# Kernel optimization log

Measured on AMD Instinct MI355X. Metric: run time of the kernel, lower is better.

The kernel has to match this reference:

```python
import jax, jax.numpy as jnp
import numpy as np

T, B, V, D, H, L, AH = 64, 128, 50000, 300, 300, 20, 300
EPS = 1e-8


def lstm_scan(x, Wih, Whh, b, h_dim):
    # x: [T, N, d_in]; PyTorch LSTM gate order i, f, g, o
    N = x.shape[1]

    def step(carry, xt):
        h, c = carry
        g = xt @ Wih.T + h @ Whh.T + b
        i, f, gg, o = jnp.split(g, 4, axis=-1)
        c = jax.nn.sigmoid(f) * c + jax.nn.sigmoid(i) * jnp.tanh(gg)
        h = jax.nn.sigmoid(o) * jnp.tanh(c)
        return (h, c), h

    init = (jnp.zeros((N, h_dim), x.dtype), jnp.zeros((N, h_dim), x.dtype))
    _, hs = jax.lax.scan(step, init, x)
    return hs  # [T, N, h_dim]


def mp_full(p, v, W):
    # p:[T,B,H], v:[B,H], W:[L,H] -> [T,B,L]; cos(W_l*p, W_l*v) via W^2 contraction
    W2 = W * W
    num = jnp.einsum('tbh,bh,lh->tbl', p, v, W2)
    pn = jnp.sqrt(jnp.einsum('tbh,lh->tbl', p * p, W2))
    vn = jnp.sqrt(jnp.einsum('bh,lh->bl', v * v, W2))
    return num / (pn * vn[None] + EPS)


def mp_elem(p, q, W):
    # p,q:[T,B,H] -> [T,B,L]
    W2 = W * W
    num = jnp.einsum('tbh,lh->tbl', p * q, W2)
    pn = jnp.sqrt(jnp.einsum('tbh,lh->tbl', p * p, W2))
    qn = jnp.sqrt(jnp.einsum('tbh,lh->tbl', q * q, W2))
    return num / (pn * qn + EPS)


def mp_pair(p, h, W):
    # p:[Tp,B,H], h:[Th,B,H] -> [Tp,Th,B,L]
    W2 = W * W
    num = jnp.einsum('tbh,sbh,lh->tsbl', p, h, W2)
    pn = jnp.sqrt(jnp.einsum('tbh,lh->tbl', p * p, W2))
    hn = jnp.sqrt(jnp.einsum('sbh,lh->sbl', h * h, W2))
    return num / (pn[:, None] * hn[None] + EPS)


def match_dir(p, h, v_full, Wf, Wm, Wa, Wma):
    full = mp_full(p, v_full, Wf)                       # full matching
    maxp = mp_pair(p, h, Wm).max(axis=1)                # maxpooling matching
    pn = p / (jnp.linalg.norm(p, axis=-1, keepdims=True) + EPS)
    hn = h / (jnp.linalg.norm(h, axis=-1, keepdims=True) + EPS)
    att = jnp.einsum('tbh,sbh->tsb', pn, hn)            # cosine attention
    w = att / (att.sum(axis=1, keepdims=True) + EPS)
    hmean = jnp.einsum('tsb,sbh->tbh', w, h)
    attm = mp_elem(p, hmean, Wa)                        # attentive matching
    idx = jnp.argmax(att, axis=1)                       # [Tp,B]
    hmax = h[idx, jnp.arange(h.shape[1])]               # [Tp,B,H]
    maxattm = mp_elem(p, hmax, Wma)                     # max-attentive matching
    return jnp.concatenate([full, maxp, attm, maxattm], axis=-1)


def multi_perspective(p_fw, p_bw, h_fw, h_bw, mp_W):
    m_fw = match_dir(p_fw, h_fw, h_fw[-1], mp_W[0], mp_W[1], mp_W[2], mp_W[3])
    m_bw = match_dir(p_bw, h_bw, h_bw[0], mp_W[4], mp_W[5], mp_W[6], mp_W[7])
    return jnp.concatenate([m_fw, m_bw], axis=-1)  # [T,B,8L]


def setup_inputs() -> dict:
    key = jax.random.key(0)
    ks = jax.random.split(key, 20)
    s = 0.05
    return {
        'premise': jax.random.randint(ks[0], (T, B), 0, V),
        'hypothesis': jax.random.randint(ks[1], (T, B), 0, V),
        'embed_W': jax.random.normal(ks[2], (V, D), jnp.float32),
        'cell_Wih': jax.random.normal(ks[3], (4 * H, D), jnp.float32) * s,
        'cell_Whh': jax.random.normal(ks[4], (4 * H, H), jnp.float32) * s,
        'cell_b': jax.random.normal(ks[5], (4 * H,), jnp.float32) * s,
        'mp_W': jax.random.normal(ks[6], (8, L, H), jnp.float32),
        'agg_Wih_f': jax.random.normal(ks[7], (4 * AH, 16 * L), jnp.float32) * s,
        'agg_Whh_f': jax.random.normal(ks[8], (4 * AH, AH), jnp.float32) * s,
        'agg_b_f': jax.random.normal(ks[9], (4 * AH,), jnp.float32) * s,
        'agg_Wih_b': jax.random.normal(ks[10], (4 * AH, 16 * L), jnp.float32) * s,
        'agg_Whh_b': jax.random.normal(ks[11], (4 * AH, AH), jnp.float32) * s,
        'agg_b_b': jax.random.normal(ks[12], (4 * AH,), jnp.float32) * s,
        'bn_gamma': jnp.ones((3, 2 * AH), jnp.float32),
        'bn_beta': jnp.zeros((3, 2 * AH), jnp.float32),
        'mlp_W1': jax.random.normal(ks[13], (2 * AH, 2 * AH), jnp.float32) * s,
        'mlp_b1': jax.random.normal(ks[14], (2 * AH,), jnp.float32) * s,
        'mlp_W2': jax.random.normal(ks[15], (2 * AH, 2 * AH), jnp.float32) * s,
        'mlp_b2': jax.random.normal(ks[16], (2 * AH,), jnp.float32) * s,
        'out_W': jax.random.normal(ks[17], (3, 2 * AH), jnp.float32) * s,
        'out_b': jax.random.normal(ks[18], (3,), jnp.float32) * s,
    }


def reference(premise, hypothesis, embed_W, cell_Wih, cell_Whh, cell_b, mp_W,
              agg_Wih_f, agg_Whh_f, agg_b_f, agg_Wih_b, agg_Whh_b, agg_b_b,
              bn_gamma, bn_beta, mlp_W1, mlp_b1, mlp_W2, mlp_b2, out_W, out_b):
    p = embed_W[premise]                      # [T,B,D]
    h = embed_W[hypothesis]                   # [T,B,D]
    comb = jnp.concatenate([p, h], axis=1)    # [T,2B,D] (premise|hypothesis along batch)
    hs_fw = lstm_scan(comb, cell_Wih, cell_Whh, cell_b, H)
    hs_bw = lstm_scan(comb[::-1], cell_Wih, cell_Whh, cell_b, H)[::-1]  # time-aligned
    p_fw, h_fw = hs_fw[:, :B], hs_fw[:, B:]
    p_bw, h_bw = hs_bw[:, :B], hs_bw[:, B:]
    m_ph = multi_perspective(p_fw, p_bw, h_fw, h_bw, mp_W)
    m_hp = multi_perspective(h_fw, h_bw, p_fw, p_bw, mp_W)
    m = jnp.concatenate([m_ph, m_hp], axis=-1)  # [T,B,16L]
    a_f = lstm_scan(m, agg_Wih_f, agg_Whh_f, agg_b_f, AH)[-1]
    a_b = lstm_scan(m[::-1], agg_Wih_b, agg_Whh_b, agg_b_b, AH)[-1]
    x = jnp.concatenate([a_f, a_b], axis=-1)    # [B, 2*AH]
    inv = np.float32(1.0 / np.sqrt(1.0 + 1e-5))  # eval-mode BN, running stats (0,1)
    bn = lambda z, i: bn_gamma[i] * z * inv + bn_beta[i]
    x = jax.nn.relu(bn(x, 0) @ mlp_W1.T + mlp_b1)
    x = jax.nn.relu(bn(x, 1) @ mlp_W2.T + mlp_b2)
    return bn(x, 2) @ out_W.T + out_b           # [B, 3]
```

## Files before the change

kernel.cpp:

```cpp
#include <hip/hip_runtime.h>
#include <cstddef>
#include <cstdint>
#include <math.h>

#define EPSF 1e-8f


typedef _Float16 half8v __attribute__((ext_vector_type(8)));
typedef float f32x4v __attribute__((ext_vector_type(4)));
union U4H8 { uint4 u; half8v h; _Float16 e[8]; };

__device__ __forceinline__ float fsig(float x) {
  float e = __expf(-x);
  return __builtin_amdgcn_rcpf(1.f + e);
}
__device__ __forceinline__ float ftanh(float x) {
  float e = __expf(-2.f * fabsf(x));
  float r = (1.f - e) * __builtin_amdgcn_rcpf(1.f + e);
  return copysignf(r, x);
}

__device__ __forceinline__ uint4 gld16(const uint4* p) {
  uint4 r;
  asm volatile("global_load_dwordx4 %0, %1, off" : "=v"(r) : "v"(p));
  return r;
}

#define GMM_LDS_BYTES (2 * (128 * 72 * 2) + 2 * (240 * 72 * 2))

__global__ __launch_bounds__(512, 1) void gemm_mfma_nt(
    const float* __restrict__ A, const float* __restrict__ B,
    const float* __restrict__ bias, float* __restrict__ C,
    int M, int K)
{
  extern __shared__ char smem[];
  _Float16* Ah = (_Float16*)smem;
  _Float16* Al = (_Float16*)(smem + 18432);
  _Float16* Bh = (_Float16*)(smem + 36864);
  _Float16* Bl = (_Float16*)(smem + 36864 + 34560);

  const int tid = threadIdx.x;
  const int wv = tid >> 6, lane = tid & 63;
  const int lm = lane & 15, lg = lane >> 4;
  const int mbase = blockIdx.y << 7;
  const int nbase = blockIdx.x * 240;

  f32x4v acc[15];
#pragma unroll
  for (int nt = 0; nt < 15; nt++) acc[nt] = (f32x4v){0.f, 0.f, 0.f, 0.f};

  const int nchunk = (K + 63) >> 6;
  for (int c = 0; c < nchunk; c++) {
    const int kc = c << 6;
    for (int e = tid; e < 2048; e += 512) {
      int row = e >> 4, q = e & 15;
      int k = kc + q * 4;
      const float* src = A + (size_t)(mbase + row) * K;
      float4 v = make_float4(0.f, 0.f, 0.f, 0.f);
      if (k + 4 <= K) {
        v = *(const float4*)(src + k);
      } else {
        if (k + 0 < K) v.x = src[k + 0];
        if (k + 1 < K) v.y = src[k + 1];
        if (k + 2 < K) v.z = src[k + 2];
        if (k + 3 < K) v.w = src[k + 3];
      }
      _Float16 hx = (_Float16)v.x, hy = (_Float16)v.y,
               hz = (_Float16)v.z, hw = (_Float16)v.w;
      _Float16* d = &Ah[row * 72 + q * 4];
      d[0] = hx; d[1] = hy; d[2] = hz; d[3] = hw;
      _Float16* dl = &Al[row * 72 + q * 4];
      dl[0] = (_Float16)(v.x - (float)hx); dl[1] = (_Float16)(v.y - (float)hy);
      dl[2] = (_Float16)(v.z - (float)hz); dl[3] = (_Float16)(v.w - (float)hw);
    }
    for (int e = tid; e < 3840; e += 512) {
      int row = e >> 4, q = e & 15;
      int k = kc + q * 4;
      const float* src = B + (size_t)(nbase + row) * K;
      float4 v = make_float4(0.f, 0.f, 0.f, 0.f);
      if (k + 4 <= K) {
        v = *(const float4*)(src + k);
      } else {
        if (k + 0 < K) v.x = src[k + 0];
        if (k + 1 < K) v.y = src[k + 1];
        if (k + 2 < K) v.z = src[k + 2];
        if (k + 3 < K) v.w = src[k + 3];
      }
      _Float16 hx = (_Float16)v.x, hy = (_Float16)v.y,
               hz = (_Float16)v.z, hw = (_Float16)v.w;
      _Float16* d = &Bh[row * 72 + q * 4];
      d[0] = hx; d[1] = hy; d[2] = hz; d[3] = hw;
      _Float16* dl = &Bl[row * 72 + q * 4];
      dl[0] = (_Float16)(v.x - (float)hx); dl[1] = (_Float16)(v.y - (float)hy);
      dl[2] = (_Float16)(v.z - (float)hz); dl[3] = (_Float16)(v.w - (float)hw);
    }
    __syncthreads();

#pragma unroll
    for (int kt = 0; kt < 2; kt++) {
      U4H8 ah, al;
      ah.u = *(const uint4*)&Ah[(wv * 16 + lm) * 72 + kt * 32 + lg * 8];
      al.u = *(const uint4*)&Al[(wv * 16 + lm) * 72 + kt * 32 + lg * 8];
#pragma unroll
      for (int nt = 0; nt < 15; nt++) {
        U4H8 bh, bl;
        bh.u = *(const uint4*)&Bh[(nt * 16 + lm) * 72 + kt * 32 + lg * 8];
        bl.u = *(const uint4*)&Bl[(nt * 16 + lm) * 72 + kt * 32 + lg * 8];
        acc[nt] = __builtin_amdgcn_mfma_f32_16x16x32_f16(ah.h, bh.h, acc[nt], 0, 0, 0);
        acc[nt] = __builtin_amdgcn_mfma_f32_16x16x32_f16(al.h, bh.h, acc[nt], 0, 0, 0);
        acc[nt] = __builtin_amdgcn_mfma_f32_16x16x32_f16(ah.h, bl.h, acc[nt], 0, 0, 0);
      }
    }
    __syncthreads();
  }

#pragma unroll
  for (int nt = 0; nt < 15; nt++) {
    int col = nbase + nt * 16 + lm;
    float bv = bias[col];
#pragma unroll
    for (int r = 0; r < 4; r++) {
      int m = mbase + wv * 16 + lg * 4 + r;
      C[(size_t)m * 1200 + col] = acc[nt][r] + bv;
    }
  }
}

__global__ __launch_bounds__(256) void permW_kernel(
    const float* __restrict__ W, const float* __restrict__ bias,
    float* __restrict__ Wp, float* __restrict__ bp, int K)
{
  int r = blockIdx.x;
  int gate = r & 3, u = r >> 2;
  int src = gate * 300 + u;
  const float* s = W + (size_t)src * K;
  float* d = Wp + (size_t)r * K;
  for (int c = threadIdx.x; c < K; c += 256) d[c] = s[c];
  if (threadIdx.x == 0) bp[r] = bias[src];
}

__global__ __launch_bounds__(256) void packB_kernel(
    const float* __restrict__ W0, const float* __restrict__ W1,
    const float* __restrict__ W2,
    uint4* __restrict__ T0, uint4* __restrict__ T1, uint4* __restrict__ T2)
{
  int i = blockIdx.x * 256 + threadIdx.x;
  if (i >= 48000) return;
  const float* W = (blockIdx.y == 0) ? W0 : (blockIdx.y == 1) ? W1 : W2;
  uint4* T = (blockIdx.y == 0) ? T0 : (blockIdx.y == 1) ? T1 : T2;
  int lane = i & 63;
  int tile = i >> 6;
  int nt = tile / 10, kt = tile - nt * 10;
  int lm = lane & 15, lg = lane >> 4;
  int colp = nt * 16 + lm;
  int u = colp >> 2, gate = colp & 3;
  int n = gate * 300 + u;
  U4H8 v;
#pragma unroll
  for (int j = 0; j < 8; j++) {
    int k = kt * 32 + lg * 8 + j;
    float x = (k < 300) ? W[(size_t)n * 300 + k] : 0.f;
    v.e[j] = (_Float16)x;
  }
  T[i] = v.u;
}

#define LSTM_LDS_BYTES (5248 + 38528 + 11 * 10240)

__global__ __launch_bounds__(512, 2) void lstm_res(
    const uint4* WB0, const uint4* WB1,
    const float* __restrict__ gx0, const float* __restrict__ gx1,
    float* hist0, float* hist1,
    float* hfin,
    int NB)
{
  extern __shared__ char smem[];
  _Float16* hA8 = (_Float16*)smem;
  float* gsh = (float*)(smem + 5248);
  uint4* bls = (uint4*)(smem + 5248 + 38528);

  const int b = blockIdx.x;
  const int xcd = b & 7;
  const int grp = b >> 3;
  const int dirb = xcd >> 2;
  const int n0 = (grp * 4 + (xcd & 3)) * 8;
  const int tid = threadIdx.x;
  const int wv = tid >> 6, lane = tid & 63;
  const int lm = lane & 15, lg = lane >> 4;

  const uint4* WB = dirb ? WB1 : WB0;
  const float* gx = dirb ? gx1 : gx0;
  float* hist = dirb ? hist1 : hist0;

  U4H8 br0[10], br1[10];
  {
    const uint4* p0 = WB + (size_t)(wv * 10) * 64 + lane;
    const uint4* p1 = WB + (size_t)((wv + 8) * 10) * 64 + lane;
#pragma unroll
    for (int kt = 0; kt < 10; kt++) br0[kt].u = gld16(p0 + kt * 64);
#pragma unroll
    for (int kt = 0; kt < 10; kt++) br1[kt].u = gld16(p1 + kt * 64);
  }
  for (int e = tid; e < 7040; e += 512) bls[e] = WB[16 * 640 + e];
  for (int e = tid; e < 8 * 328; e += 512) hA8[e] = (_Float16)0.f;
  asm volatile("s_waitcnt vmcnt(0)" ::: "memory");
  __builtin_amdgcn_sched_barrier(0);
  __syncthreads();

  int gxo[5], gsho[5], hAo[5], ho[5];
  bool act[5];
#pragma unroll
  for (int q = 0; q < 5; q++) {
    int e = tid + q * 512;
    act[q] = (e < 2400);
    int m = act[q] ? (e / 300) : 0;
    int u = act[q] ? (e - m * 300) : 0;
    gxo[q] = (n0 + m) * 1200 + 4 * u;
    gsho[q] = m * 1204 + 4 * u;
    hAo[q] = m * 328 + u;
    ho[q] = (n0 + m) * 300 + u;
  }

  float crs[5] = {0.f, 0.f, 0.f, 0.f, 0.f};

  for (int t = 0; t < 64; t++) {
    const int tg = dirb ? (63 - t) : t;
    const size_t gxstep = (size_t)tg * NB * 1200;

    float4 gxv[5];
#pragma unroll
    for (int q = 0; q < 5; q++) {
      gxv[q] = make_float4(0.f, 0.f, 0.f, 0.f);
      if (act[q]) gxv[q] = *(const float4*)(gx + gxstep + gxo[q]);
    }

    uint4 bA[5], bB[5];
#pragma unroll
    for (int kt = 0; kt < 5; kt++)
      bA[kt] = WB[(size_t)((27 + wv) * 10 + kt) * 64 + lane];

    U4H8 af[10];
#pragma unroll
    for (int kt = 0; kt < 10; kt++) {
      uint4 v = make_uint4(0u, 0u, 0u, 0u);
      if (lm < 8) v = *(const uint4*)&hA8[lm * 328 + kt * 32 + lg * 8];
      af[kt].u = v;
    }

    {
      f32x4v a0 = {0.f, 0.f, 0.f, 0.f};
      f32x4v a1 = {0.f, 0.f, 0.f, 0.f};
#pragma unroll
      for (int kt = 0; kt < 5; kt++)
        a0 = __builtin_amdgcn_mfma_f32_16x16x32_f16(af[kt].h, br0[kt].h, a0, 0, 0, 0);
#pragma unroll
      for (int kt = 5; kt < 10; kt++)
        a1 = __builtin_amdgcn_mfma_f32_16x16x32_f16(af[kt].h, br0[kt].h, a1, 0, 0, 0);
      if (lg < 2) {
        int col = wv * 16 + lm;
#pragma unroll
        for (int r = 0; r < 4; r++)
          gsh[(lg * 4 + r) * 1204 + col] = a0[r] + a1[r];
      }
    }
    {
      f32x4v a0 = {0.f, 0.f, 0.f, 0.f};
      f32x4v a1 = {0.f, 0.f, 0.f, 0.f};
#pragma unroll
      for (int kt = 0; kt < 5; kt++)
        a0 = __builtin_amdgcn_mfma_f32_16x16x32_f16(af[kt].h, br1[kt].h, a0, 0, 0, 0);
#pragma unroll
      for (int kt = 5; kt < 10; kt++)
        a1 = __builtin_amdgcn_mfma_f32_16x16x32_f16(af[kt].h, br1[kt].h, a1, 0, 0, 0);
      if (lg < 2) {
        int col = (wv + 8) * 16 + lm;
#pragma unroll
        for (int r = 0; r < 4; r++)
          gsh[(lg * 4 + r) * 1204 + col] = a0[r] + a1[r];
      }
    }

#pragma unroll 1
    for (int i = 0; i < 6; i++) {
      int nt = 27 + wv + 8 * i;
#pragma unroll
      for (int kt = 0; kt < 5; kt++)
        bB[kt] = WB[(size_t)(nt * 10 + 5 + kt) * 64 + lane];
      f32x4v a0 = {0.f, 0.f, 0.f, 0.f};
#pragma unroll
      for (int kt = 0; kt < 5; kt++) {
        U4H8 bb; bb.u = bA[kt];
        a0 = __builtin_amdgcn_mfma_f32_16x16x32_f16(af[kt].h, bb.h, a0, 0, 0, 0);
      }
      if (i + 1 < 6) {
#pragma unroll
        for (int kt = 0; kt < 5; kt++)
          bA[kt] = WB[(size_t)((nt + 8) * 10 + kt) * 64 + lane];
      }
      f32x4v a1 = {0.f, 0.f, 0.f, 0.f};
#pragma unroll
      for (int kt = 0; kt < 5; kt++) {
        U4H8 bb; bb.u = bB[kt];
        a1 = __builtin_amdgcn_mfma_f32_16x16x32_f16(af[5 + kt].h, bb.h, a1, 0, 0, 0);
      }
      if (lg < 2) {
        int col = nt * 16 + lm;
#pragma unroll
        for (int r = 0; r < 4; r++)
          gsh[(lg * 4 + r) * 1204 + col] = a0[r] + a1[r];
      }
    }

#pragma unroll 1
    for (int li = 0; li < 2; li++) {
      int idxL = li == 0 ? wv : (8 + wv);
      if (li == 1 && wv >= 3) break;
      const uint4* bt = &bls[idxL * 640];
      f32x4v a0 = {0.f, 0.f, 0.f, 0.f};
      f32x4v a1 = {0.f, 0.f, 0.f, 0.f};
#pragma unroll
      for (int kt = 0; kt < 5; kt++) {
        U4H8 bb; bb.u = bt[kt * 64 + lane];
        a0 = __builtin_amdgcn_mfma_f32_16x16x32_f16(af[kt].h, bb.h, a0, 0, 0, 0);
      }
#pragma unroll
      for (int kt = 5; kt < 10; kt++) {
        U4H8 bb; bb.u = bt[kt * 64 + lane];
        a1 = __builtin_amdgcn_mfma_f32_16x16x32_f16(af[kt].h, bb.h, a1, 0, 0, 0);
      }
      if (lg < 2) {
        int col = (16 + idxL) * 16 + lm;
#pragma unroll
        for (int r = 0; r < 4; r++)
          gsh[(lg * 4 + r) * 1204 + col] = a0[r] + a1[r];
      }
    }
    __syncthreads();

#pragma unroll
    for (int q = 0; q < 5; q++) {
      if (act[q]) {
        const float4 gs = *(const float4*)&gsh[gsho[q]];
        float gi = gxv[q].x + gs.x;
        float gf = gxv[q].y + gs.y;
        float gg = gxv[q].z + gs.z;
        float go = gxv[q].w + gs.w;
        float si = fsig(gi);
        float sf = fsig(gf);
        float so = fsig(go);
        float cc = sf * crs[q] + si * ftanh(gg);
        float h = so * ftanh(cc);
        crs[q] = cc;
        hA8[hAo[q]] = (_Float16)h;
        if (hist) hist[(size_t)tg * NB * 300 + ho[q]] = h;
        if (hfin && t == 63) hfin[(size_t)dirb * NB * 300 + ho[q]] = h;
      }
    }
    __syncthreads();
  }
}

__global__ void embed_kernel(
    const int* __restrict__ prem, const int* __restrict__ hyp,
    const float* __restrict__ embW, float* __restrict__ comb)
{
  size_t i = (size_t)blockIdx.x * 256 + threadIdx.x;
  if (i >= (size_t)64 * 256 * 75) return;
  int d4 = (int)(i % 75);
  size_t r = i / 75;
  int n = (int)(r % 256);
  int t = (int)(r / 256);
  int id = (n < 128) ? prem[t * 128 + n] : hyp[t * 128 + (n - 128)];
  float4 v = *(const float4*)(embW + (size_t)id * 300 + d4 * 4);
  *(float4*)(comb + ((size_t)t * 256 + n) * 300 + d4 * 4) = v;
}

__global__ __launch_bounds__(320) void norm4_kernel(
    const float* __restrict__ hs_fw, const float* __restrict__ hs_bw,
    const float* __restrict__ mp_W,
    float* __restrict__ nm4, float* __restrict__ pnorm)
{
  const int t = blockIdx.x, n = blockIdx.y, dir = blockIdx.z;
  const float* HS = dir ? hs_bw : hs_fw;
  const float* row = HS + ((size_t)t * 256 + n) * 300;
  __shared__ float sh[300];
  const int tid = threadIdx.x, g = tid >> 4, lane = tid & 15;
  for (int k = tid; k < 300; k += 320) sh[k] = row[k];
  __syncthreads();
  if (g == 0) {
    float s2 = 0.f;
    for (int k = lane; k < 300; k += 16) { float x = sh[k]; s2 += x * x; }
    for (int o = 8; o; o >>= 1) s2 += __shfl_down(s2, o, 16);
    if (lane == 0) pnorm[((size_t)dir * 64 + t) * 256 + n] = sqrtf(s2);
  }
#pragma unroll
  for (int wset = 0; wset < 4; wset++) {
    const float* W = mp_W + dir * 24000 + wset * 6000 + g * 300;
    float s1 = 0.f;
    for (int k = lane; k < 300; k += 16) {
      float x = sh[k];
      float w = W[k];
      s1 += x * x * w * w;
    }
    for (int o = 8; o; o >>= 1) s1 += __shfl_down(s1, o, 16);
    if (lane == 0)
      nm4[((((size_t)dir * 4 + wset) * 64 + t) * 256 + n) * 20 + g] = sqrtf(s1);
  }
}

__global__ __launch_bounds__(256) void att_kernel(
    const float* __restrict__ hs_fw, const float* __restrict__ hs_bw,
    const float* __restrict__ pnorm,
    float* __restrict__ watt, int* __restrict__ idxbuf)
{
  const int b = blockIdx.x, z = blockIdx.y;
  const int dir = z & 1;
  const float* HS = dir ? hs_bw : hs_fw;
  const int p_n = (z < 2) ? b : 128 + b;
  const int h_n = (z < 2) ? 128 + b : b;
  const float* pnD = pnorm + (size_t)dir * 16384;

  __shared__ float pch[64 * 100];
  __shared__ float hch[64 * 100];
  __shared__ float att[64 * 65];
  __shared__ float winv_sh[64];

  const int tid = threadIdx.x;
  const int i = tid >> 4, j = tid & 15;
  float acc[4][4];
#pragma unroll
  for (int a = 0; a < 4; a++)
#pragma unroll
    for (int c = 0; c < 4; c++) acc[a][c] = 0.f;

  for (int kc = 0; kc < 300; kc += 100) {
    for (int e = tid; e < 1600; e += 256) {
      int row = e / 25, kq = e - row * 25;
      float4 v = *(const float4*)(HS + ((size_t)row * 256 + p_n) * 300 + kc + kq * 4);
      *(float4*)&pch[row * 100 + kq * 4] = v;
      float4 w = *(const float4*)(HS + ((size_t)row * 256 + h_n) * 300 + kc + kq * 4);
      *(float4*)&hch[row * 100 + kq * 4] = w;
    }
    __syncthreads();
#pragma unroll 5
    for (int kq = 0; kq < 25; kq++) {
      float4 av[4], bv[4];
#pragma unroll
      for (int a = 0; a < 4; a++) av[a] = *(const float4*)&pch[(i + 16 * a) * 100 + kq * 4];
#pragma unroll
      for (int c = 0; c < 4; c++) bv[c] = *(const float4*)&hch[(j + 16 * c) * 100 + kq * 4];
#pragma unroll
      for (int a = 0; a < 4; a++)
#pragma unroll
        for (int c = 0; c < 4; c++)
          acc[a][c] += av[a].x * bv[c].x + av[a].y * bv[c].y + av[a].z * bv[c].z + av[a].w * bv[c].w;
    }
    __syncthreads();
  }

#pragma unroll
  for (int a = 0; a < 4; a++) {
    int t = i + 16 * a;
    float pn = pnD[t * 256 + p_n] + EPSF;
#pragma unroll
    for (int c = 0; c < 4; c++) {
      int s = j + 16 * c;
      float hn = pnD[s * 256 + h_n] + EPSF;
      att[t * 65 + s] = acc[a][c] / (pn * hn);
    }
  }
  __syncthreads();
  if (tid < 64) {
    int t = tid;
    float ssum = 0.f, mx = -1e30f; int mi = 0;
    for (int s = 0; s < 64; s++) {
      float a = att[t * 65 + s];
      ssum += a;
      if (a > mx) { mx = a; mi = s; }
    }
    winv_sh[t] = 1.f / (ssum + EPSF);
    idxbuf[((size_t)z * 128 + b) * 64 + t] = mi;
  }
  __syncthreads();
  for (int e = tid; e < 4096; e += 256) {
    int t = e >> 6, s = e & 63;
    watt[((size_t)z * 128 + b) * 4096 + t * 64 + s] = att[t * 65 + s] * winv_sh[t];
  }
}

__global__ __launch_bounds__(256) void hmean_kernel(
    const float* __restrict__ hs_fw, const float* __restrict__ hs_bw,
    const float* __restrict__ watt, float* __restrict__ hmeanbuf)
{
  const int b = blockIdx.x, z = blockIdx.y;
  const int dir = z & 1;
  const float* HS = dir ? hs_bw : hs_fw;
  const int h_n = (z < 2) ? 128 + b : b;

  __shared__ float wsh[64 * 65];
  __shared__ float hch[64 * 128];

  const int tid = threadIdx.x;
  const int ti = tid >> 4, kj = tid & 15;
  const float* wsrc = watt + ((size_t)z * 128 + b) * 4096;
  for (int e = tid; e < 4096; e += 256) {
    int t = e >> 6, s = e & 63;
    wsh[t * 65 + s] = wsrc[t * 64 + s];
  }

  for (int kbase = 0; kbase < 300; kbase += 128) {
    int kw = min(128, 300 - kbase);
    int nf4 = kw >> 2;
    __syncthreads();
    for (int e = tid; e < 64 * nf4; e += 256) {
      int row = e / nf4, q = e - row * nf4;
      float4 v = *(const float4*)(HS + ((size_t)row * 256 + h_n) * 300 + kbase + q * 4);
      *(float4*)&hch[row * 128 + q * 4] = v;
    }
    __syncthreads();
    float acc[4][8];
#pragma unroll
    for (int a = 0; a < 4; a++)
#pragma unroll
      for (int c = 0; c < 8; c++) acc[a][c] = 0.f;
    for (int s = 0; s < 64; s++) {
      float4 h0 = *(const float4*)&hch[s * 128 + 4 * kj];
      float4 h1 = *(const float4*)&hch[s * 128 + 4 * (kj + 16)];
#pragma unroll
      for (int a = 0; a < 4; a++) {
        float w = wsh[(4 * ti + a) * 65 + s];
        acc[a][0] += w * h0.x; acc[a][1] += w * h0.y; acc[a][2] += w * h0.z; acc[a][3] += w * h0.w;
        acc[a][4] += w * h1.x; acc[a][5] += w * h1.y; acc[a][6] += w * h1.z; acc[a][7] += w * h1.w;
      }
    }
#pragma unroll
    for (int a = 0; a < 4; a++) {
      int t = 4 * ti + a;
#pragma unroll
      for (int c = 0; c < 2; c++) {
        int kq = kj + 16 * c;
        if (kq * 4 < kw) {
          int k = kbase + kq * 4;
          float4 v = make_float4(acc[a][4 * c], acc[a][4 * c + 1], acc[a][4 * c + 2], acc[a][4 * c + 3]);
          *(float4*)&hmeanbuf[(((size_t)z * 128 + b) * 64 + t) * 300 + k] = v;
        }
      }
    }
  }
}

#define MAXP_LDS_BYTES (41984 + 41984 + 13120 + 5120 + 5120)

__global__ __launch_bounds__(512, 2) void maxp_mfma(
    const float* __restrict__ hs_fw, const float* __restrict__ hs_bw,
    const float* __restrict__ mp_W, const float* __restrict__ nm4,
    float* __restrict__ m_out)
{
  extern __shared__ char smem[];
  _Float16* pA = (_Float16*)smem;
  _Float16* hB = (_Float16*)(smem + 41984);
  _Float16* w2h = (_Float16*)(smem + 83968);
  float* pn_sh = (float*)(smem + 97088);
  float* hn_sh = (float*)(smem + 102208);

  const int b = blockIdx.x, z = blockIdx.y;
  const int dir = z & 1;
  const float* HS = dir ? hs_bw : hs_fw;
  const int p_n = (z < 2) ? b : 128 + b;
  const int h_n = (z < 2) ? 128 + b : b;
  const float* Wm = mp_W + dir * 24000 + 6000;
  const float* nmD = nm4 + ((size_t)dir * 4 + 1) * 327680;

  const int tid = threadIdx.x;
  const int wv = tid >> 6, lane = tid & 63;
  const int lm = lane & 15, lg = lane >> 4;

  for (int e = tid; e < 4800; e += 512) {
    int row = e / 75, q = e - row * 75;
    float4 v = *(const float4*)(HS + ((size_t)row * 256 + p_n) * 300 + q * 4);
    float4 w = *(const float4*)(HS + ((size_t)row * 256 + h_n) * 300 + q * 4);
    _Float16* pd = &pA[row * 328 + q * 4];
    pd[0] = (_Float16)v.x; pd[1] = (_Float16)v.y; pd[2] = (_Float16)v.z; pd[3] = (_Float16)v.w;
    _Float16* hd = &hB[row * 328 + q * 4];
    hd[0] = (_Float16)w.x; hd[1] = (_Float16)w.y; hd[2] = (_Float16)w.z; hd[3] = (_Float16)w.w;
  }
  for (int e = tid; e < 64 * 28; e += 512) {
    int row = e / 28, c = 300 + (e - row * 28);
    pA[row * 328 + c] = (_Float16)0.f;
    hB[row * 328 + c] = (_Float16)0.f;
  }
  for (int e = tid; e < 1500; e += 512) {
    int row = e / 75, q = e - row * 75;
    float4 w = *(const float4*)(Wm + (size_t)row * 300 + q * 4);
    _Float16* d = &w2h[row * 328 + q * 4];
    d[0] = (_Float16)(w.x * w.x); d[1] = (_Float16)(w.y * w.y);
    d[2] = (_Float16)(w.z * w.z); d[3] = (_Float16)(w.w * w.w);
  }
  for (int e = tid; e < 20 * 28; e += 512) {
    int row = e / 28, c = 300 + (e - row * 28);
    w2h[row * 328 + c] = (_Float16)0.f;
  }
  for (int e = tid; e < 1280; e += 512) {
    int tq = e / 20, l = e - tq * 20;
    pn_sh[e] = nmD[((size_t)tq * 256 + p_n) * 20 + l];
    hn_sh[e] = nmD[((size_t)tq * 256 + h_n) * 20 + l];
  }
  __syncthreads();

  float rmax[10][4];
#pragma unroll
  for (int i = 0; i < 10; i++)
#pragma unroll
    for (int r = 0; r < 4; r++) rmax[i][r] = -1e30f;

#pragma unroll
  for (int sp = 0; sp < 2; sp++) {
    U4H8 hf[2][10];
#pragma unroll
    for (int hh = 0; hh < 2; hh++)
#pragma unroll
      for (int kt = 0; kt < 10; kt++)
        hf[hh][kt].u = *(const uint4*)&hB[(sp * 32 + hh * 16 + lm) * 328 + kt * 32 + lg * 8];

#pragma unroll
    for (int i = 0; i < 10; i++) {
      int xt = wv + 8 * i;
      int l = xt >> 2, t0 = (xt & 3) << 4;
      U4H8 af[10];
#pragma unroll
      for (int kt = 0; kt < 10; kt++) {
        U4H8 pf, wf;
        pf.u = *(const uint4*)&pA[(t0 + lm) * 328 + kt * 32 + lg * 8];
        wf.u = *(const uint4*)&w2h[l * 328 + kt * 32 + lg * 8];
        af[kt].h = pf.h * wf.h;
      }
      float pnv[4];
#pragma unroll
      for (int r = 0; r < 4; r++) pnv[r] = pn_sh[(t0 + lg * 4 + r) * 20 + l];
#pragma unroll
      for (int hh = 0; hh < 2; hh++) {
        int st = sp * 2 + hh;
        f32x4v acc = {0.f, 0.f, 0.f, 0.f};
#pragma unroll
        for (int kt = 0; kt < 10; kt++)
          acc = __builtin_amdgcn_mfma_f32_16x16x32_f16(af[kt].h, hf[hh][kt].h, acc, 0, 0, 0);
        float hn = hn_sh[(st * 16 + lm) * 20 + l];
#pragma unroll
        for (int r = 0; r < 4; r++) {
          float val = acc[r] * __builtin_amdgcn_rcpf(pnv[r] * hn + EPSF);
          rmax[i][r] = fmaxf(rmax[i][r], val);
        }
      }
    }
  }

#pragma unroll
  for (int i = 0; i < 10; i++) {
    int xt = wv + 8 * i;
    int l = xt >> 2, t0 = (xt & 3) << 4;
#pragma unroll
    for (int r = 0; r < 4; r++) {
      float v = rmax[i][r];
#pragma unroll
      for (int off = 8; off; off >>= 1) v = fmaxf(v, __shfl_down(v, off, 16));
      if (lm == 0) {
        int t = t0 + lg * 4 + r;
        m_out[((size_t)t * 128 + b) * 320 + z * 80 + 20 + l] = v;
      }
    }
  }
}

__global__ __launch_bounds__(320) void rest_kernel(
    const float* __restrict__ hs_fw, const float* __restrict__ hs_bw,
    const float* __restrict__ mp_W, const float* __restrict__ nm4,
    const float* __restrict__ hmeanbuf, const int* __restrict__ idxbuf,
    float* __restrict__ m_out)
{
  const int b = blockIdx.x, z = blockIdx.y;
  const int dir = z & 1;
  const float* HS = dir ? hs_bw : hs_fw;
  const int p_n = (z < 2) ? b : 128 + b;
  const int h_n = (z < 2) ? 128 + b : b;
  const int v_t = dir ? 0 : 63;

  __shared__ float w2f[6000], w2a[6000], w2m[6000];
  __shared__ float vsh[300], psh[300], hmsh[300], hxsh[300];

  const int tid = threadIdx.x;
  const int g = tid >> 4, lane = tid & 15;
  const float* Wf = mp_W + dir * 24000;
  const float* Wa = Wf + 12000;
  const float* Wma = Wf + 18000;
  for (int e = tid; e < 6000; e += 320) {
    float a = Wf[e], bb = Wa[e], c = Wma[e];
    w2f[e] = a * a; w2a[e] = bb * bb; w2m[e] = c * c;
  }
  for (int e = tid; e < 300; e += 320)
    vsh[e] = HS[((size_t)v_t * 256 + h_n) * 300 + e];
  __syncthreads();

  const float* base0 = nm4 + ((size_t)dir * 4 + 0) * 327680;
  const float* base2 = nm4 + ((size_t)dir * 4 + 2) * 327680;
  const float* base3 = nm4 + ((size_t)dir * 4 + 3) * 327680;
  const float vnf = base0[((size_t)v_t * 256 + h_n) * 20 + g];

  for (int t = 0; t < 64; t++) {
    int idx = idxbuf[((size_t)z * 128 + b) * 64 + t];
    __syncthreads();
    for (int e = tid; e < 300; e += 320) {
      psh[e] = HS[((size_t)t * 256 + p_n) * 300 + e];
      hmsh[e] = hmeanbuf[(((size_t)z * 128 + b) * 64 + t) * 300 + e];
      hxsh[e] = HS[((size_t)idx * 256 + h_n) * 300 + e];
    }
    __syncthreads();
    float nf = 0.f, na = 0.f, qa = 0.f, nm = 0.f;
#pragma unroll
    for (int c = 0; c < 5; c++) {
      int k4 = lane + 16 * c;
      if (k4 < 75) {
        float4 p = *(const float4*)&psh[4 * k4];
        float4 v = *(const float4*)&vsh[4 * k4];
        float4 hm = *(const float4*)&hmsh[4 * k4];
        float4 hx = *(const float4*)&hxsh[4 * k4];
        float4 wf = *(const float4*)&w2f[g * 300 + 4 * k4];
        float4 wa = *(const float4*)&w2a[g * 300 + 4 * k4];
        float4 wm = *(const float4*)&w2m[g * 300 + 4 * k4];
        nf += p.x * v.x * wf.x + p.y * v.y * wf.y + p.z * v.z * wf.z + p.w * v.w * wf.w;
        na += p.x * hm.x * wa.x + p.y * hm.y * wa.y + p.z * hm.z * wa.z + p.w * hm.w * wa.w;
        qa += hm.x * hm.x * wa.x + hm.y * hm.y * wa.y + hm.z * hm.z * wa.z + hm.w * hm.w * wa.w;
        nm += p.x * hx.x * wm.x + p.y * hx.y * wm.y + p.z * hx.z * wm.z + p.w * hx.w * wm.w;
      }
    }
#pragma unroll
    for (int o = 8; o; o >>= 1) {
      nf += __shfl_down(nf, o);
      na += __shfl_down(na, o);
      qa += __shfl_down(qa, o);
      nm += __shfl_down(nm, o);
    }
    if (lane == 0) {
      float pnf = base0[((size_t)t * 256 + p_n) * 20 + g];
      float pna = base2[((size_t)t * 256 + p_n) * 20 + g];
      float pnm = base3[((size_t)t * 256 + p_n) * 20 + g];
      float qnm = base3[((size_t)idx * 256 + h_n) * 20 + g];
      float* mrow = m_out + ((size_t)t * 128 + b) * 320 + z * 80;
      mrow[g] = nf / (pnf * vnf + EPSF);
      mrow[40 + g] = na / (pna * sqrtf(qa) + EPSF);
      mrow[60 + g] = nm / (pnm * qnm + EPSF);
    }
  }
}

__global__ __launch_bounds__(256) void mlp_kernel(
    const float* __restrict__ shA0, const float* __restrict__ shA1,
    const float* __restrict__ bnG, const float* __restrict__ bnB,
    const float* __restrict__ W1, const float* __restrict__ b1,
    const float* __restrict__ W2, const float* __restrict__ b2,
    const float* __restrict__ outW, const float* __restrict__ outb,
    float* __restrict__ out)
{
  const int b = blockIdx.x;
  const int tid = threadIdx.x;
  __shared__ float x0[600], x1[600];
  const float inv = 1.0f / sqrtf(1.0f + 1e-5f);
  for (int j = tid; j < 600; j += 256) {
    float v = (j < 300) ? shA0[b * 300 + j] : shA1[b * 300 + (j - 300)];
    x0[j] = bnG[j] * v * inv + bnB[j];
  }
  __syncthreads();
  for (int j = tid; j < 600; j += 256) {
    float acc = b1[j];
    const float* w = W1 + (size_t)j * 600;
    for (int k = 0; k < 600; k++) acc += x0[k] * w[k];
    float r = fmaxf(acc, 0.f);
    x1[j] = bnG[600 + j] * r * inv + bnB[600 + j];
  }
  __syncthreads();
  for (int j = tid; j < 600; j += 256) {
    float acc = b2[j];
    const float* w = W2 + (size_t)j * 600;
    for (int k = 0; k < 600; k++) acc += x1[k] * w[k];
    float r = fmaxf(acc, 0.f);
    x0[j] = bnG[1200 + j] * r * inv + bnB[1200 + j];
  }
  __syncthreads();
  if (tid < 3) {
    float acc = outb[tid];
    const float* w = outW + tid * 600;
    for (int k = 0; k < 600; k++) acc += x0[k] * w[k];
    out[b * 3 + tid] = acc;
  }
}

extern "C" void kernel_launch(void* const* d_in, const int* in_sizes, int n_in,
                              void* d_out, int out_size, void* d_ws, size_t ws_size,
                              hipStream_t stream) {
  const int* premise = (const int*)d_in[0];
  const int* hypothesis = (const int*)d_in[1];
  const float* embW = (const float*)d_in[2];
  const float* cWih = (const float*)d_in[3];
  const float* cWhh = (const float*)d_in[4];
  const float* cb = (const float*)d_in[5];
  const float* mpW = (const float*)d_in[6];
  const float* aWihF = (const float*)d_in[7];
  const float* aWhhF = (const float*)d_in[8];
  const float* abF = (const float*)d_in[9];
  const float* aWihB = (const float*)d_in[10];
  const float* aWhhB = (const float*)d_in[11];
  const float* abB = (const float*)d_in[12];
  const float* bnG = (const float*)d_in[13];
  const float* bnB = (const float*)d_in[14];
  const float* W1 = (const float*)d_in[15];
  const float* b1 = (const float*)d_in[16];
  const float* W2 = (const float*)d_in[17];
  const float* b2 = (const float*)d_in[18];
  const float* outW = (const float*)d_in[19];
  const float* outb = (const float*)d_in[20];
  float* out = (float*)d_out;

  float* ws = (float*)d_ws;
  float* comb  = ws + 0;
  float* gates = ws + 4915200;
  float* hsfw  = ws + 24576000;
  float* hsbw  = ws + 29491200;
  float* pnorm = ws + 34406400;
  float* mbuf  = ws + 35094528;
  float* sha   = ws + 38023168;

  uint4* WBctx = (uint4*)comb;
  uint4* WBaf  = (uint4*)(comb + 192000);
  uint4* WBab  = (uint4*)(comb + 384000);
  float* aWihFP = comb + 576000;
  float* aWihBP = comb + 960000;
  float* abFP   = comb + 1344000;
  float* abBP   = comb + 1345200;

  float* cWihP = hsfw;
  float* cbP   = hsfw + 360000;

  float* watt     = gates;
  float* hmeanbuf = gates + 2097152;
  int*   idxbuf   = (int*)(gates + 11927552);
  float* nm4      = gates + 11960320;

  hipFuncSetAttribute((const void*)lstm_res,
                      hipFuncAttributeMaxDynamicSharedMemorySize, LSTM_LDS_BYTES);
  hipFuncSetAttribute((const void*)maxp_mfma,
                      hipFuncAttributeMaxDynamicSharedMemorySize, MAXP_LDS_BYTES);
  hipFuncSetAttribute((const void*)gemm_mfma_nt,
                      hipFuncAttributeMaxDynamicSharedMemorySize, GMM_LDS_BYTES);

  embed_kernel<<<dim3(4800), dim3(256), 0, stream>>>(premise, hypothesis, embW, comb);
  permW_kernel<<<dim3(1200), dim3(256), 0, stream>>>(cWih, cb, cWihP, cbP, 300);

  gemm_mfma_nt<<<dim3(5, 128), dim3(512), GMM_LDS_BYTES, stream>>>(
      comb, cWihP, cbP, gates, 16384, 300);

  packB_kernel<<<dim3(188, 3), dim3(256), 0, stream>>>(
      cWhh, aWhhF, aWhhB, WBctx, WBaf, WBab);
  permW_kernel<<<dim3(1200), dim3(256), 0, stream>>>(aWihF, abF, aWihFP, abFP, 320);
  permW_kernel<<<dim3(1200), dim3(256), 0, stream>>>(aWihB, abB, aWihBP, abBP, 320);

  lstm_res<<<dim3(64), dim3(512), LSTM_LDS_BYTES, stream>>>(
      WBctx, WBctx, gates, gates, hsfw, hsbw, nullptr, 256);

  norm4_kernel<<<dim3(64, 256, 2), dim3(320), 0, stream>>>(hsfw, hsbw, mpW, nm4, pnorm);

  att_kernel<<<dim3(128, 4), dim3(256), 0, stream>>>(hsfw, hsbw, pnorm, watt, idxbuf);
  hmean_kernel<<<dim3(128, 4), dim3(256), 0, stream>>>(hsfw, hsbw, watt, hmeanbuf);
  maxp_mfma<<<dim3(128, 4), dim3(512), MAXP_LDS_BYTES, stream>>>(
      hsfw, hsbw, mpW, nm4, mbuf);
  rest_kernel<<<dim3(128, 4), dim3(320), 0, stream>>>(hsfw, hsbw, mpW, nm4, hmeanbuf, idxbuf, mbuf);

  float* gaf = gates;
  float* gab = gates + 9830400;
  gemm_mfma_nt<<<dim3(5, 64), dim3(512), GMM_LDS_BYTES, stream>>>(
      mbuf, aWihFP, abFP, gaf, 8192, 320);
  gemm_mfma_nt<<<dim3(5, 64), dim3(512), GMM_LDS_BYTES, stream>>>(
      mbuf, aWihBP, abBP, gab, 8192, 320);

  lstm_res<<<dim3(32), dim3(512), LSTM_LDS_BYTES, stream>>>(
      WBaf, WBab, gaf, gab, nullptr, nullptr, sha, 128);

  mlp_kernel<<<dim3(128), dim3(256), 0, stream>>>(
      sha, sha + 38400, bnG, bnB, W1, b1, W2, b2, outW, outb, out);
}
```

Before: 1.980 ms.

## Stage squared perspective weights in LDS and loop over time per block in norm4

The norm kernel now launches one block per (sequence, direction) instead of per (time, sequence, direction). Each block squares and caches that direction's 24000 perspective weights in about 97 KB of dynamic LDS, then loops over all 64 time steps, reusing the cached W^2 instead of rereading the weights from global memory for every row. The cost is a much smaller grid (512 blocks of 320 threads), heavy LDS use that limits occupancy, and a serial time loop with two barriers per step. Row loads are no longer overlapped with compute.

```diff
diff --git a/kernel.cpp b/kernel.cpp
--- a/kernel.cpp
+++ b/kernel.cpp
@@ -375,36 +375,51 @@
   *(float4*)(comb + ((size_t)t * 256 + n) * 300 + d4 * 4) = v;
 }
 
+#define NORM4_LDS_BYTES (96000 + 1216)
+
 __global__ __launch_bounds__(320) void norm4_kernel(
     const float* __restrict__ hs_fw, const float* __restrict__ hs_bw,
     const float* __restrict__ mp_W,
     float* __restrict__ nm4, float* __restrict__ pnorm)
 {
-  const int t = blockIdx.x, n = blockIdx.y, dir = blockIdx.z;
+  extern __shared__ char nsm[];
+  float* w2sh = (float*)nsm;
+  float* sh = (float*)(nsm + 96000);
+
+  const int n = blockIdx.x, dir = blockIdx.y;
   const float* HS = dir ? hs_bw : hs_fw;
-  const float* row = HS + ((size_t)t * 256 + n) * 300;
-  __shared__ float sh[300];
   const int tid = threadIdx.x, g = tid >> 4, lane = tid & 15;
-  for (int k = tid; k < 300; k += 320) sh[k] = row[k];
+
+  const float* Wd = mp_W + dir * 24000;
+  for (int e = tid; e < 24000; e += 320) {
+    float w = Wd[e];
+    w2sh[e] = w * w;
+  }
   __syncthreads();
-  if (g == 0) {
-    float s2 = 0.f;
-    for (int k = lane; k < 300; k += 16) { float x = sh[k]; s2 += x * x; }
-    for (int o = 8; o; o >>= 1) s2 += __shfl_down(s2, o, 16);
-    if (lane == 0) pnorm[((size_t)dir * 64 + t) * 256 + n] = sqrtf(s2);
-  }
-#pragma unroll
-  for (int wset = 0; wset < 4; wset++) {
-    const float* W = mp_W + dir * 24000 + wset * 6000 + g * 300;
-    float s1 = 0.f;
-    for (int k = lane; k < 300; k += 16) {
-      float x = sh[k];
-      float w = W[k];
-      s1 += x * x * w * w;
-    }
-    for (int o = 8; o; o >>= 1) s1 += __shfl_down(s1, o, 16);
-    if (lane == 0)
-      nm4[((((size_t)dir * 4 + wset) * 64 + t) * 256 + n) * 20 + g] = sqrtf(s1);
+
+  for (int t = 0; t < 64; t++) {
+    for (int k = tid; k < 300; k += 320)
+      sh[k] = HS[((size_t)t * 256 + n) * 300 + k];
+    __syncthreads();
+    if (g == 0) {
+      float s2 = 0.f;
+      for (int k = lane; k < 300; k += 16) { float x = sh[k]; s2 += x * x; }
+      for (int o = 8; o; o >>= 1) s2 += __shfl_down(s2, o, 16);
+      if (lane == 0) pnorm[((size_t)dir * 64 + t) * 256 + n] = sqrtf(s2);
+    }
+#pragma unroll
+    for (int wset = 0; wset < 4; wset++) {
+      const float* W2 = w2sh + wset * 6000 + g * 300;
+      float s1 = 0.f;
+      for (int k = lane; k < 300; k += 16) {
+        float x = sh[k];
+        s1 += x * x * W2[k];
+      }
+      for (int o = 8; o; o >>= 1) s1 += __shfl_down(s1, o, 16);
+      if (lane == 0)
+        nm4[((((size_t)dir * 4 + wset) * 64 + t) * 256 + n) * 20 + g] = sqrtf(s1);
+    }
+    __syncthreads();
   }
 }
 
@@ -850,6 +865,8 @@
                       hipFuncAttributeMaxDynamicSharedMemorySize, MAXP_LDS_BYTES);
   hipFuncSetAttribute((const void*)gemm_mfma_nt,
                       hipFuncAttributeMaxDynamicSharedMemorySize, GMM_LDS_BYTES);
+  hipFuncSetAttribute((const void*)norm4_kernel,
+                      hipFuncAttributeMaxDynamicSharedMemorySize, NORM4_LDS_BYTES);
 
   embed_kernel<<<dim3(4800), dim3(256), 0, stream>>>(premise, hypothesis, embW, comb);
   permW_kernel<<<dim3(1200), dim3(256), 0, stream>>>(cWih, cb, cWihP, cbP, 300);
@@ -865,7 +882,8 @@
   lstm_res<<<dim3(64), dim3(512), LSTM_LDS_BYTES, stream>>>(
       WBctx, WBctx, gates, gates, hsfw, hsbw, nullptr, 256);
 
-  norm4_kernel<<<dim3(64, 256, 2), dim3(320), 0, stream>>>(hsfw, hsbw, mpW, nm4, pnorm);
+  norm4_kernel<<<dim3(256, 2), dim3(320), NORM4_LDS_BYTES, stream>>>(
+      hsfw, hsbw, mpW, nm4, pnorm);
 
   att_kernel<<<dim3(128, 4), dim3(256), 0, stream>>>(hsfw, hsbw, pnorm, watt, idxbuf);
   hmean_kernel<<<dim3(128, 4), dim3(256), 0, stream>>>(hsfw, hsbw, watt, hmeanbuf);
```

Result: slower. 2.405 ms (+21.4%).
